# Optimization experiments

Measured on AMD Instinct MI355X. Metric: run time of the kernel, lower is better.

Reference implementation:

```python
import math
from functools import lru_cache
import numpy as np
import jax, jax.numpy as jnp

# ---------------- CG coefficient precompute (mirrors torch-gauge) ----------------

def _fact(n):
    return math.factorial(n)


def _cg_complex(j1, m1, j2, m2, j, m):
    """Clebsch-Gordan coefficient <j1 m1 j2 m2 | j m> for integer l (Racah formula)."""
    if m1 + m2 != m:
        return 0.0
    if j < abs(j1 - j2) or j > j1 + j2:
        return 0.0
    pre = math.sqrt((2 * j + 1) * _fact(j1 + j2 - j) * _fact(j1 - j2 + j)
                    * _fact(-j1 + j2 + j) / _fact(j1 + j2 + j + 1))
    pre *= math.sqrt(_fact(j1 + m1) * _fact(j1 - m1) * _fact(j2 + m2)
                     * _fact(j2 - m2) * _fact(j + m) * _fact(j - m))
    kmin = max(0, j2 - j - m1, j1 + m2 - j)
    kmax = min(j1 + j2 - j, j1 - m1, j2 + m2)
    s = 0.0
    for k in range(kmin, kmax + 1):
        s += (-1) ** k / (_fact(k) * _fact(j1 + j2 - j - k) * _fact(j1 - m1 - k)
                          * _fact(j2 + m2 - k) * _fact(j - j2 + m1 + k) * _fact(j - j1 - m2 + k))
    return pre * s


def _csh_to_rsh(l):
    """Unitary complex->real spherical harmonics transform, columns = real m."""
    A = np.zeros((2 * l + 1, 2 * l + 1), dtype=np.complex128)
    s2 = 1.0 / math.sqrt(2.0)
    for m in range(-l, l + 1):
        if m < 0:
            A[l + m, l + m] = 1j * s2
            A[l - m, l + m] = -1j * ((-1) ** m) * s2
        elif m == 0:
            A[l, l] = 1.0
        else:
            A[l + m, l + m] = ((-1) ** m) * s2
            A[l - m, l + m] = s2
    return A


@lru_cache(maxsize=None)
def _rsh_cg_compact(j1, j2, j):
    """Real-SH CG coefficients in compact [4, nnz] form: (m1, m2, m, coeff)."""
    csh = np.zeros((2 * j1 + 1, 2 * j2 + 1, 2 * j + 1))
    for m1 in range(-j1, j1 + 1):
        for m2 in range(-j2, j2 + 1):
            m = m1 + m2
            if -j <= m <= j:
                csh[j1 + m1, j2 + m2, j + m] = _cg_complex(j1, m1, j2, m2, j, m)
    rsh = np.einsum('abc,ai,bj,ck->ijk', csh.astype(np.complex128),
                    _csh_to_rsh(j1), _csh_to_rsh(j2), np.conj(_csh_to_rsh(j)))
    rsh = np.real(rsh * ((-1j) ** (j1 + j2 + j)))
    m1s, m2s, ms = np.meshgrid(np.arange(-j1, j1 + 1), np.arange(-j2, j2 + 1),
                               np.arange(-j, j + 1), indexing='ij')
    mask = np.abs(rsh) > 1e-12
    return np.stack([m1s[mask], m2s[mask], ms[mask], rsh[mask]], axis=0)


def _build_coupler(md1, md2, parity=0, overlap_out=True, trunc_in=True):
    """Replicates CGCoupler._init_params: builds cg_tilde and gather/scatter indices."""
    md1 = np.asarray(md1, dtype=np.int64)
    md2 = np.asarray(md2, dtype=np.int64)
    md_in = np.stack([md1, md2])
    max_n_out = np.maximum(md1, md2)
    L = md_in.shape[1]
    n_irreps = np.arange(L) * 2 + 1
    off_in = np.cumsum(md_in * n_irreps[None, :], axis=1)
    off_in = np.concatenate([np.zeros((2, 1), dtype=np.int64), off_in[:, :-1]], axis=1)
    max_l = L - 1
    metadata_out = np.zeros_like(max_n_out)
    valid = []
    for lout in range(max_l + 1):
        for l1 in range(max_l + 1):
            for l2 in range(max_l + 1):
                cp = (-1) ** (lout + l1 + l2)
                if parity != 0 and parity != cp:
                    continue
                if l1 + l2 < lout or abs(l1 - l2) > lout:
                    continue
                if trunc_in:
                    if l1 + l2 > max_l:
                        continue
                    deg = int(min(md_in[0, l1], md_in[1, l2], max_n_out[l1 + l2]))
                else:
                    deg = int(min(md_in[0, l1], md_in[1, l2], max_n_out[lout]))
                if not overlap_out:
                    metadata_out[lout] += deg
                elif deg > metadata_out[lout]:
                    metadata_out[lout] = deg
                if deg > 0:
                    valid.append((lout, l1, l2, deg))
    off_out = np.cumsum(metadata_out * n_irreps)
    off_out = np.concatenate([[0], off_out[:-1]]).astype(np.int64)
    cg_tilde, r1, r2, ro = [], [], [], []
    ns_off, lout_last = 0, 0
    for lout, l1, l2, deg in valid:
        if lout > lout_last:
            ns_off = 0
        src = _rsh_cg_compact(l1, l2, lout)  # [4, nnz]
        seg = np.repeat(src, deg, axis=1)    # repeat_interleave along columns
        ns = np.tile(np.arange(deg), src.shape[1])
        r1.append(off_in[0, l1] + (seg[0] + l1) * md_in[0, l1] + ns)
        r2.append(off_in[1, l2] + (seg[1] + l2) * md_in[1, l2] + ns)
        ro.append(off_out[lout] + (seg[2] + lout) * metadata_out[lout] + ns_off + ns)
        cg_tilde.append(seg[3])
        if not overlap_out:
            ns_off += deg
        lout_last = lout
    out_dim = int(np.sum(metadata_out * n_irreps))
    return (np.concatenate(cg_tilde).astype(np.float32),
            np.concatenate(r1).astype(np.int64),
            np.concatenate(r2).astype(np.int64),
            np.concatenate(ro).astype(np.int64),
            out_dim)


METADATA = [64, 64, 32, 32]  # lmax=3, rep_dim = 64 + 192 + 160 + 224 = 640
N_BATCH = 16384


def setup_inputs() -> dict:
    key = jax.random.key(0)
    k1, k2 = jax.random.split(key)
    cg, r1, r2, ro, out_dim = _build_coupler(METADATA, METADATA,
                                             parity=0, overlap_out=True, trunc_in=True)
    rep_dim = int(np.sum(np.asarray(METADATA) * (np.arange(len(METADATA)) * 2 + 1)))
    x1 = jax.random.normal(k1, (N_BATCH, rep_dim), dtype=jnp.float32)
    x2 = jax.random.normal(k2, (N_BATCH, rep_dim), dtype=jnp.float32)
    return {
        'x1': x1, 'x2': x2,
        'cg_tilde': jnp.asarray(cg),
        'repids_in1': jnp.asarray(r1),
        'repids_in2': jnp.asarray(r2),
        'repids_out': jnp.asarray(ro),
        'out_dim': out_dim,
    }


def reference(x1, x2, cg_tilde, repids_in1, repids_in2, repids_out, out_dim):
    # gather -> multiply by CG coefficients -> scatter-add along the rep dim
    out_tilde = x1[:, repids_in1] * x2[:, repids_in2] * cg_tilde[None, :]  # [N, M]
    out = jnp.zeros((x1.shape[0], out_dim), dtype=x1.dtype)
    return out.at[:, repids_out].add(out_tilde)
```

## Files before the change

kernel.cpp:

```cpp
#include <hip/hip_runtime.h>
#include <cstddef>


#define BLOCK 256


constexpr double cfact(int n) { double r = 1; for (int i = 2; i <= n; ++i) r *= i; return r; }

constexpr double csqrt_(double x) {
    if (x <= 0) return 0;
    double g = x;
    for (int i = 0; i < 80; ++i) g = 0.5 * (g + x / g);
    return g;
}

constexpr double cg_complex(int j1, int m1, int j2, int m2, int j, int m) {
    if (m1 + m2 != m) return 0;
    int dj = (j1 - j2 < 0) ? (j2 - j1) : (j1 - j2);
    if (j < dj || j > j1 + j2) return 0;
    double pre = csqrt_((2 * j + 1) * cfact(j1 + j2 - j) * cfact(j1 - j2 + j)
                        * cfact(-j1 + j2 + j) / cfact(j1 + j2 + j + 1));
    pre *= csqrt_(cfact(j1 + m1) * cfact(j1 - m1) * cfact(j2 + m2)
                  * cfact(j2 - m2) * cfact(j + m) * cfact(j - m));
    int kmin = 0;
    if (j2 - j - m1 > kmin) kmin = j2 - j - m1;
    if (j1 + m2 - j > kmin) kmin = j1 + m2 - j;
    int kmax = j1 + j2 - j;
    if (j1 - m1 < kmax) kmax = j1 - m1;
    if (j2 + m2 < kmax) kmax = j2 + m2;
    double s = 0;
    for (int k = kmin; k <= kmax; ++k) {
        double t = 1.0 / (cfact(k) * cfact(j1 + j2 - j - k) * cfact(j1 - m1 - k)
                          * cfact(j2 + m2 - k) * cfact(j - j2 + m1 + k) * cfact(j - j1 - m2 + k));
        s += (k & 1) ? -t : t;
    }
    return pre * s;
}

struct CD { double re, im; };
constexpr CD cmul(CD a, CD b) { return {a.re * b.re - a.im * b.im, a.re * b.im + a.im * b.re}; }

constexpr CD A_ent(int l, int a, int col) {
    const double s2 = 0.70710678118654752440;
    int m = col - l, mp = a - l;
    if (m < 0) {
        double sgn = ((-m) & 1) ? -1.0 : 1.0;
        if (mp == m)  return {0.0, s2};
        if (mp == -m) return {0.0, -sgn * s2};
        return {0.0, 0.0};
    } else if (m == 0) {
        return (mp == 0) ? CD{1.0, 0.0} : CD{0.0, 0.0};
    } else {
        double sgn = (m & 1) ? -1.0 : 1.0;
        if (mp == m)  return {sgn * s2, 0.0};
        if (mp == -m) return {s2, 0.0};
        return {0.0, 0.0};
    }
}

constexpr double rsh_cg(int j1, int j2, int j, int i, int jj, int k) {
    double re = 0, im = 0;
    for (int m1 = -j1; m1 <= j1; ++m1)
        for (int m2 = -j2; m2 <= j2; ++m2) {
            int m = m1 + m2;
            if (m < -j || m > j) continue;
            double c = cg_complex(j1, m1, j2, m2, j, m);
            if (c == 0) continue;
            CD a1 = A_ent(j1, j1 + m1, i);
            CD a2 = A_ent(j2, j2 + m2, jj);
            CD a3 = A_ent(j, j + m, k);
            a3.im = -a3.im;
            CD p = cmul(cmul(a1, a2), a3);
            re += c * p.re;
            im += c * p.im;
        }
    int ph = (j1 + j2 + j) & 3;
    if (ph == 0) return re;
    if (ph == 1) return im;
    if (ph == 2) return -re;
    return -im;
}


template <int L1, int L2, int LO, int IDX, int NT>
__device__ __forceinline__ void terms_rec(const float (&x1v)[16], const float (&x2v)[16],
                                          float (&acc)[16]) {
    if constexpr (IDX < NT) {
        constexpr int N2 = 2 * L2 + 1, NO = 2 * LO + 1;
        constexpr int u1 = IDX / (N2 * NO);
        constexpr int u2 = (IDX / NO) % N2;
        constexpr int uo = IDX % NO;
        constexpr double v = rsh_cg(L1, L2, LO, u1, u2, uo);
        constexpr float cgv = (v > 1e-12 || v < -1e-12) ? (float)v : 0.0f;
        constexpr int SB1 = (L1 == 0) ? 0 : (L1 == 1) ? 1 : (L1 == 2) ? 4 : 9;
        constexpr int SB2 = (L2 == 0) ? 0 : (L2 == 1) ? 1 : (L2 == 2) ? 4 : 9;
        constexpr int SBO = (LO == 0) ? 0 : (LO == 1) ? 1 : (LO == 2) ? 4 : 9;
        if constexpr (cgv != 0.0f) {
            acc[SBO + uo] += cgv * x1v[SB1 + u1] * x2v[SB2 + u2];
        }
        terms_rec<L1, L2, LO, IDX + 1, NT>(x1v, x2v, acc);
    }
}

template <int L1, int L2, int LO>
__device__ __forceinline__ void proc_block(const float (&x1v)[16], const float (&x2v)[16],
                                           float (&acc)[16]) {
    terms_rec<L1, L2, LO, 0, (2 * L1 + 1) * (2 * L2 + 1) * (2 * LO + 1)>(x1v, x2v, acc);
}


__device__ __forceinline__ float ntload(const float* p) {
    return __builtin_nontemporal_load(p);
}

__global__ __launch_bounds__(BLOCK) void cg_main_kernel(
    const float* __restrict__ x1, const float* __restrict__ x2,
    float* __restrict__ out, int N)
{
    const int gid = blockIdx.x * BLOCK + threadIdx.x;
    const int row = gid >> 6;
    const int c   = gid & 63;
    if (row >= N) return;

    const float* p1 = x1 + (size_t)row * 640;
    const float* p2 = x2 + (size_t)row * 640;

    float x1v[16], x2v[16], acc[16];
#pragma unroll
    for (int i = 0; i < 16; ++i) acc[i] = 0.f;

    x1v[0] = ntload(p1 + c);
    x2v[0] = ntload(p2 + c);
#pragma unroll
    for (int u = 0; u < 3; ++u) {
        x1v[1 + u] = ntload(p1 + 64 + u * 64 + c);
        x2v[1 + u] = ntload(p2 + 64 + u * 64 + c);
    }
    const bool lo32 = (c < 32);
    if (lo32) {
#pragma unroll
        for (int u = 0; u < 5; ++u) {
            x1v[4 + u] = ntload(p1 + 256 + u * 32 + c);
            x2v[4 + u] = ntload(p2 + 256 + u * 32 + c);
        }
#pragma unroll
        for (int u = 0; u < 7; ++u) {
            x1v[9 + u] = ntload(p1 + 416 + u * 32 + c);
            x2v[9 + u] = ntload(p2 + 416 + u * 32 + c);
        }
    }

    proc_block<0, 0, 0>(x1v, x2v, acc);
    proc_block<0, 1, 1>(x1v, x2v, acc);
    proc_block<1, 0, 1>(x1v, x2v, acc);

    if (lo32) {
        proc_block<1, 1, 0>(x1v, x2v, acc);
        proc_block<1, 1, 1>(x1v, x2v, acc);
        proc_block<1, 2, 1>(x1v, x2v, acc);
        proc_block<2, 1, 1>(x1v, x2v, acc);
        proc_block<0, 2, 2>(x1v, x2v, acc);
        proc_block<2, 0, 2>(x1v, x2v, acc);
        proc_block<1, 1, 2>(x1v, x2v, acc);
        proc_block<1, 2, 2>(x1v, x2v, acc);
        proc_block<2, 1, 2>(x1v, x2v, acc);
        proc_block<0, 3, 3>(x1v, x2v, acc);
        proc_block<3, 0, 3>(x1v, x2v, acc);
        proc_block<1, 2, 3>(x1v, x2v, acc);
        proc_block<2, 1, 3>(x1v, x2v, acc);
    }

    float* po = out + (size_t)row * 640;
    __builtin_nontemporal_store(acc[0], po + c);
#pragma unroll
    for (int u = 0; u < 3; ++u)
        __builtin_nontemporal_store(acc[1 + u], po + 64 + u * 64 + c);
    if (lo32) {
#pragma unroll
        for (int u = 0; u < 5; ++u)
            __builtin_nontemporal_store(acc[4 + u], po + 256 + u * 32 + c);
#pragma unroll
        for (int u = 0; u < 7; ++u)
            __builtin_nontemporal_store(acc[9 + u], po + 416 + u * 32 + c);
    }
}

extern "C" void kernel_launch(void* const* d_in, const int* in_sizes, int n_in,
                              void* d_out, int out_size, void* d_ws, size_t ws_size,
                              hipStream_t stream) {
    const float* x1 = (const float*)d_in[0];
    const float* x2 = (const float*)d_in[1];
    float* out = (float*)d_out;

    const int N = in_sizes[0] / 640;

    const int total_threads = N * 64;
    cg_main_kernel<<<(total_threads + BLOCK - 1) / BLOCK, BLOCK, 0, stream>>>(
        x1, x2, out, N);
}
```

Baseline: 130.4 us.

## Map two rows per wavefront with 32 lanes each to remove divergence

Each wavefront now handles two rows, with 32 lanes per row. Each lane processes both the full channel set for its lane and the extra l0/l1 channels (t+32), instead of half the lanes idling through the l>=2 work. This removes the lo32 branch divergence and halves the thread count. It also replaces the nontemporal loads with plain loads. In exchange each thread carries more registers and more work, which may lower occupancy.

```diff
diff --git a/kernel.cpp b/kernel.cpp
--- a/kernel.cpp
+++ b/kernel.cpp
@@ -83,8 +83,9 @@
 
 
 template <int L1, int L2, int LO, int IDX, int NT>
-__device__ __forceinline__ void terms_rec(const float (&x1v)[16], const float (&x2v)[16],
-                                          float (&acc)[16]) {
+__device__ __forceinline__ void terms_rec(const float* __restrict__ x1v,
+                                          const float* __restrict__ x2v,
+                                          float* __restrict__ acc) {
     if constexpr (IDX < NT) {
         constexpr int N2 = 2 * L2 + 1, NO = 2 * LO + 1;
         constexpr int u1 = IDX / (N2 * NO);
@@ -103,86 +104,90 @@
 }
 
 template <int L1, int L2, int LO>
-__device__ __forceinline__ void proc_block(const float (&x1v)[16], const float (&x2v)[16],
-                                           float (&acc)[16]) {
+__device__ __forceinline__ void proc_block(const float* __restrict__ x1v,
+                                           const float* __restrict__ x2v,
+                                           float* __restrict__ acc) {
     terms_rec<L1, L2, LO, 0, (2 * L1 + 1) * (2 * L2 + 1) * (2 * LO + 1)>(x1v, x2v, acc);
 }
 
-
-__device__ __forceinline__ float ntload(const float* p) {
-    return __builtin_nontemporal_load(p);
-}
 
 __global__ __launch_bounds__(BLOCK) void cg_main_kernel(
     const float* __restrict__ x1, const float* __restrict__ x2,
     float* __restrict__ out, int N)
 {
-    const int gid = blockIdx.x * BLOCK + threadIdx.x;
-    const int row = gid >> 6;
-    const int c   = gid & 63;
+    const int gid  = blockIdx.x * BLOCK + threadIdx.x;
+    const int wave = gid >> 6;
+    const int lane = gid & 63;
+    const int sub  = lane >> 5;
+    const int t    = lane & 31;
+    const int row  = wave * 2 + sub;
     if (row >= N) return;
 
     const float* p1 = x1 + (size_t)row * 640;
     const float* p2 = x2 + (size_t)row * 640;
 
-    float x1v[16], x2v[16], acc[16];
-#pragma unroll
-    for (int i = 0; i < 16; ++i) acc[i] = 0.f;
-
-    x1v[0] = ntload(p1 + c);
-    x2v[0] = ntload(p2 + c);
+    float x1t[16], x2t[16], acct[16];
+    float x1u[4],  x2u[4],  accu[4];
+#pragma unroll
+    for (int i = 0; i < 16; ++i) acct[i] = 0.f;
+#pragma unroll
+    for (int i = 0; i < 4; ++i) accu[i] = 0.f;
+
+    x1t[0] = p1[t];       x2t[0] = p2[t];
+    x1u[0] = p1[t + 32];  x2u[0] = p2[t + 32];
 #pragma unroll
     for (int u = 0; u < 3; ++u) {
-        x1v[1 + u] = ntload(p1 + 64 + u * 64 + c);
-        x2v[1 + u] = ntload(p2 + 64 + u * 64 + c);
-    }
-    const bool lo32 = (c < 32);
-    if (lo32) {
-#pragma unroll
-        for (int u = 0; u < 5; ++u) {
-            x1v[4 + u] = ntload(p1 + 256 + u * 32 + c);
-            x2v[4 + u] = ntload(p2 + 256 + u * 32 + c);
-        }
-#pragma unroll
-        for (int u = 0; u < 7; ++u) {
-            x1v[9 + u] = ntload(p1 + 416 + u * 32 + c);
-            x2v[9 + u] = ntload(p2 + 416 + u * 32 + c);
-        }
-    }
-
-    proc_block<0, 0, 0>(x1v, x2v, acc);
-    proc_block<0, 1, 1>(x1v, x2v, acc);
-    proc_block<1, 0, 1>(x1v, x2v, acc);
-
-    if (lo32) {
-        proc_block<1, 1, 0>(x1v, x2v, acc);
-        proc_block<1, 1, 1>(x1v, x2v, acc);
-        proc_block<1, 2, 1>(x1v, x2v, acc);
-        proc_block<2, 1, 1>(x1v, x2v, acc);
-        proc_block<0, 2, 2>(x1v, x2v, acc);
-        proc_block<2, 0, 2>(x1v, x2v, acc);
-        proc_block<1, 1, 2>(x1v, x2v, acc);
-        proc_block<1, 2, 2>(x1v, x2v, acc);
-        proc_block<2, 1, 2>(x1v, x2v, acc);
-        proc_block<0, 3, 3>(x1v, x2v, acc);
-        proc_block<3, 0, 3>(x1v, x2v, acc);
-        proc_block<1, 2, 3>(x1v, x2v, acc);
-        proc_block<2, 1, 3>(x1v, x2v, acc);
-    }
+        x1t[1 + u] = p1[64 + u * 64 + t];
+        x2t[1 + u] = p2[64 + u * 64 + t];
+        x1u[1 + u] = p1[64 + u * 64 + t + 32];
+        x2u[1 + u] = p2[64 + u * 64 + t + 32];
+    }
+#pragma unroll
+    for (int u = 0; u < 5; ++u) {
+        x1t[4 + u] = p1[256 + u * 32 + t];
+        x2t[4 + u] = p2[256 + u * 32 + t];
+    }
+#pragma unroll
+    for (int u = 0; u < 7; ++u) {
+        x1t[9 + u] = p1[416 + u * 32 + t];
+        x2t[9 + u] = p2[416 + u * 32 + t];
+    }
+
+    proc_block<0, 0, 0>(x1t, x2t, acct);
+    proc_block<0, 1, 1>(x1t, x2t, acct);
+    proc_block<1, 0, 1>(x1t, x2t, acct);
+    proc_block<0, 0, 0>(x1u, x2u, accu);
+    proc_block<0, 1, 1>(x1u, x2u, accu);
+    proc_block<1, 0, 1>(x1u, x2u, accu);
+
+    proc_block<1, 1, 0>(x1t, x2t, acct);
+    proc_block<1, 1, 1>(x1t, x2t, acct);
+    proc_block<1, 2, 1>(x1t, x2t, acct);
+    proc_block<2, 1, 1>(x1t, x2t, acct);
+    proc_block<0, 2, 2>(x1t, x2t, acct);
+    proc_block<2, 0, 2>(x1t, x2t, acct);
+    proc_block<1, 1, 2>(x1t, x2t, acct);
+    proc_block<1, 2, 2>(x1t, x2t, acct);
+    proc_block<2, 1, 2>(x1t, x2t, acct);
+    proc_block<0, 3, 3>(x1t, x2t, acct);
+    proc_block<3, 0, 3>(x1t, x2t, acct);
+    proc_block<1, 2, 3>(x1t, x2t, acct);
+    proc_block<2, 1, 3>(x1t, x2t, acct);
 
     float* po = out + (size_t)row * 640;
-    __builtin_nontemporal_store(acc[0], po + c);
-#pragma unroll
-    for (int u = 0; u < 3; ++u)
-        __builtin_nontemporal_store(acc[1 + u], po + 64 + u * 64 + c);
-    if (lo32) {
-#pragma unroll
-        for (int u = 0; u < 5; ++u)
-            __builtin_nontemporal_store(acc[4 + u], po + 256 + u * 32 + c);
-#pragma unroll
-        for (int u = 0; u < 7; ++u)
-            __builtin_nontemporal_store(acc[9 + u], po + 416 + u * 32 + c);
-    }
+    __builtin_nontemporal_store(acct[0], po + t);
+    __builtin_nontemporal_store(accu[0], po + t + 32);
+#pragma unroll
+    for (int u = 0; u < 3; ++u) {
+        __builtin_nontemporal_store(acct[1 + u], po + 64 + u * 64 + t);
+        __builtin_nontemporal_store(accu[1 + u], po + 64 + u * 64 + t + 32);
+    }
+#pragma unroll
+    for (int u = 0; u < 5; ++u)
+        __builtin_nontemporal_store(acct[4 + u], po + 256 + u * 32 + t);
+#pragma unroll
+    for (int u = 0; u < 7; ++u)
+        __builtin_nontemporal_store(acct[9 + u], po + 416 + u * 32 + t);
 }
 
 extern "C" void kernel_launch(void* const* d_in, const int* in_sizes, int n_in,
@@ -194,7 +199,7 @@
 
     const int N = in_sizes[0] / 640;
 
-    const int total_threads = N * 64;
+    const int total_threads = N * 32;
     cg_main_kernel<<<(total_threads + BLOCK - 1) / BLOCK, BLOCK, 0, stream>>>(
         x1, x2, out, N);
 }
```

New measurement: 122.7 us. -5.9%, faster.
